# Kernel optimization log

Measured on AMD Instinct MI355X. Metric: run time of the kernel, lower is better.

## Reference

```python
import jax, jax.numpy as jnp
import numpy as np

B, T, D, H = 64, 1024, 512, 1024


def setup_inputs() -> dict:
    key = jax.random.key(0)
    ks = jax.random.split(key, 9)
    s_in = 1.0 / np.sqrt(D)
    s_h = 1.0 / np.sqrt(H)
    x = jax.random.normal(ks[0], (B, T, D), dtype=jnp.float32)
    W0 = jax.random.normal(ks[1], (D, 3 * H), dtype=jnp.float32) * s_in
    U0 = jax.random.normal(ks[2], (H, 3 * H), dtype=jnp.float32) * s_h
    bi0 = jnp.zeros((3 * H,), dtype=jnp.float32)
    br0 = jnp.zeros((3 * H,), dtype=jnp.float32)
    W1 = jax.random.normal(ks[3], (D, 3 * H), dtype=jnp.float32) * s_in
    U1 = jax.random.normal(ks[4], (H, 3 * H), dtype=jnp.float32) * s_h
    bi1 = jnp.zeros((3 * H,), dtype=jnp.float32)
    br1 = jnp.zeros((3 * H,), dtype=jnp.float32)
    return {"x": x, "W0": W0, "U0": U0, "bi0": bi0, "br0": br0,
            "W1": W1, "U1": U1, "bi1": bi1, "br1": br1}


def _gru_last(x, W, U, bi, br):
    """Keras GRUCell (reset_after=True) scanned over time; returns final h [B,H]."""
    h_dim = U.shape[0]
    xT = jnp.swapaxes(x, 0, 1)  # [T, B, D]

    def step(h, xt):
        gx = xt @ W + bi          # [B, 3H] input projection + input bias
        gh = h @ U + br           # [B, 3H] recurrent projection + recurrent bias
        xz, xr, xh = jnp.split(gx, 3, axis=-1)
        hz, hr, hh = jnp.split(gh, 3, axis=-1)
        z = jax.nn.sigmoid(xz + hz)
        r = jax.nn.sigmoid(xr + hr)
        h_cand = jnp.tanh(xh + r * hh)
        h_new = z * h + (1.0 - z) * h_cand
        return h_new, None

    h0 = jnp.zeros((x.shape[0], h_dim), dtype=x.dtype)
    h_last, _ = jax.lax.scan(step, h0, xT)
    return h_last


def reference(x, W0, U0, bi0, br0, W1, U1, bi1, br1):
    out0 = _gru_last(x, W0, U0, bi0, br0)
    out1 = _gru_last(x, W1, U1, bi1, br1)
    return (out0, out1)
```

## Files before the change

kernel.cpp:

```cpp
#include <hip/hip_runtime.h>
#include <hip/hip_bf16.h>

typedef unsigned short u16;
typedef short s8v __attribute__((ext_vector_type(8)));
typedef float f4v __attribute__((ext_vector_type(4)));

#define NB 64
#define NT 1024
#define ND 512
#define NH 1024

static const size_t OFF_BAR  = 0;
static const size_t OFF_HB   = 512;
static const size_t SZ_HB    = (size_t)2*2*NB*NH*2;
static const size_t OFF_XBF  = (size_t)1<<20;
static const size_t SZ_XBF   = (size_t)NB*NT*ND*2;
static const size_t WS_FLOOR = OFF_HB + SZ_HB;
static const size_t WS_FULL  = OFF_XBF + SZ_XBF;

__device__ __forceinline__ u16 f2bf(float f) {
  union { float f; unsigned u; } v; v.f = f;
  unsigned r = v.u + 0x7fffu + ((v.u >> 16) & 1u);
  return (u16)(r >> 16);
}

__global__ void pack_x_kernel(const float* __restrict__ x, u16* __restrict__ xb) {
  long long i = (long long)blockIdx.x * 256 + threadIdx.x;
  const float4* xp = (const float4*)x;
  float4 a = xp[2*i], b = xp[2*i+1];
  s8v v;
  v[0]=(short)f2bf(a.x); v[1]=(short)f2bf(a.y); v[2]=(short)f2bf(a.z); v[3]=(short)f2bf(a.w);
  v[4]=(short)f2bf(b.x); v[5]=(short)f2bf(b.y); v[6]=(short)f2bf(b.z); v[7]=(short)f2bf(b.w);
  *((s8v*)xb + i) = v;
}

__device__ __forceinline__ void gridbar(unsigned* cnt, unsigned* gen, unsigned nb) {
  __syncthreads();
  if (threadIdx.x == 0) {
    __threadfence();
    unsigned g = __hip_atomic_load(gen, __ATOMIC_RELAXED, __HIP_MEMORY_SCOPE_AGENT);
    unsigned a = __hip_atomic_fetch_add(cnt, 1u, __ATOMIC_ACQ_REL, __HIP_MEMORY_SCOPE_AGENT);
    if (a == nb - 1u) {
      __hip_atomic_store(cnt, 0u, __ATOMIC_RELAXED, __HIP_MEMORY_SCOPE_AGENT);
      __hip_atomic_fetch_add(gen, 1u, __ATOMIC_RELEASE, __HIP_MEMORY_SCOPE_AGENT);
    } else {
      while (__hip_atomic_load(gen, __ATOMIC_ACQUIRE, __HIP_MEMORY_SCOPE_AGENT) == g)
        __builtin_amdgcn_s_sleep(2);
    }
    __threadfence();
  }
  __syncthreads();
}

template<int XBF>
__global__ void __launch_bounds__(192, 1)
rnn_persist(const float* __restrict__ xf, const u16* __restrict__ xb,
            const float* __restrict__ W0, const float* __restrict__ U0,
            const float* __restrict__ W1, const float* __restrict__ U1,
            const float* __restrict__ bi0, const float* __restrict__ br0,
            const float* __restrict__ bi1, const float* __restrict__ br1,
            u16* __restrict__ hb, unsigned* __restrict__ bar,
            float* __restrict__ out) {
  __shared__ float zr[2][64][16];
  const int tid  = threadIdx.x;
  const int lane = tid & 63;
  const int g    = tid >> 6;
  const int wg   = blockIdx.x;
  const int hd   = wg >> 6;
  const int j0   = (wg & 63) * 16;
  const int cidx = lane & 15;
  const int hi8  = (lane >> 4) << 3;
  const int q4   = (lane >> 4) << 2;

  const float* W = hd ? W1 : W0;
  const float* U = hd ? U1 : U0;
  const int col = g*1024 + j0 + cidx;

  s8v wf[16], uf[32];
  #pragma unroll
  for (int kk=0;kk<16;++kk) { s8v v;
    #pragma unroll
    for (int j=0;j<8;++j) v[j] = (short)f2bf(W[(size_t)(kk*32 + hi8 + j)*3072 + col]);
    wf[kk]=v; }
  #pragma unroll
  for (int kk=0;kk<32;++kk) { s8v v;
    #pragma unroll
    for (int j=0;j<8;++j) v[j] = (short)f2bf(U[(size_t)(kk*32 + hi8 + j)*3072 + col]);
    uf[kk]=v; }

  const float bis = (hd ? bi1 : bi0)[col];
  const float brs = (hd ? br1 : br0)[col];

  f4v hm[4];
  #pragma unroll
  for (int m=0;m<4;++m) hm[m] = f4v{0.f,0.f,0.f,0.f};

  unsigned* cnt = bar + hd*32;
  unsigned* gen = cnt + 1;

  for (int t = 0; t < NT; ++t) {
    const int p = t & 1;
    f4v cx[4], ch[4];
    #pragma unroll
    for (int m=0;m<4;++m){ cx[m]=f4v{0.f,0.f,0.f,0.f}; ch[m]=f4v{0.f,0.f,0.f,0.f}; }

    #pragma unroll
    for (int kk=0;kk<16;++kk) {
      #pragma unroll
      for (int m=0;m<4;++m) {
        s8v a;
        if (XBF) {
          a = *(const s8v*)(xb + ((size_t)((m*16+cidx)*NT + t))*ND + hi8 + kk*32);
        } else {
          const float* p4 = xf + ((size_t)((m*16+cidx)*NT + t))*ND + hi8 + kk*32;
          float4 u0 = *(const float4*)p4, u1 = *(const float4*)(p4+4);
          a[0]=(short)f2bf(u0.x); a[1]=(short)f2bf(u0.y); a[2]=(short)f2bf(u0.z); a[3]=(short)f2bf(u0.w);
          a[4]=(short)f2bf(u1.x); a[5]=(short)f2bf(u1.y); a[6]=(short)f2bf(u1.z); a[7]=(short)f2bf(u1.w);
        }
        cx[m] = __builtin_amdgcn_mfma_f32_16x16x32_bf16(a, wf[kk], cx[m], 0,0,0);
      }
    }
    const u16* hptr0 = hb + (size_t)(p*2 + hd) * (NB*NH) + (size_t)cidx*NH + hi8;
    #pragma unroll
    for (int kk=0;kk<32;++kk) {
      #pragma unroll
      for (int m=0;m<4;++m) {
        s8v a = *(const s8v*)(hptr0 + (size_t)m*16*NH + kk*32);
        ch[m] = __builtin_amdgcn_mfma_f32_16x16x32_bf16(a, uf[kk], ch[m], 0,0,0);
      }
    }

    if (g < 2) {
      #pragma unroll
      for (int m=0;m<4;++m) {
        #pragma unroll
        for (int q=0;q<4;++q) {
          float v = cx[m][q] + ch[m][q] + bis + brs;
          zr[g][m*16 + q4 + q][cidx] = 1.f/(1.f + __expf(-v));
        }
      }
    }
    __syncthreads();
    if (g == 2) {
      u16* hdst = hb + (size_t)((p^1)*2 + hd) * (NB*NH);
      #pragma unroll
      for (int m=0;m<4;++m) {
        #pragma unroll
        for (int q=0;q<4;++q) {
          int row = m*16 + q4 + q;
          float z  = zr[0][row][cidx];
          float r  = zr[1][row][cidx];
          float hc = tanhf(cx[m][q] + bis + r*(ch[m][q] + brs));
          float hn = z*hm[m][q] + (1.f - z)*hc;
          hm[m][q] = hn;
          hdst[(size_t)row*NH + j0 + cidx] = f2bf(hn);
          if (t == NT-1) out[(size_t)hd*(NB*NH) + (size_t)row*NH + j0 + cidx] = hn;
        }
      }
    }
    gridbar(cnt, gen, 64u);
  }
}

extern "C" void kernel_launch(void* const* d_in, const int* in_sizes, int n_in,
                              void* d_out, int out_size, void* d_ws, size_t ws_size,
                              hipStream_t stream) {
  const float* x   = (const float*)d_in[0];
  const float* W0  = (const float*)d_in[1];
  const float* U0  = (const float*)d_in[2];
  const float* bi0 = (const float*)d_in[3];
  const float* br0 = (const float*)d_in[4];
  const float* W1  = (const float*)d_in[5];
  const float* U1  = (const float*)d_in[6];
  const float* bi1 = (const float*)d_in[7];
  const float* br1 = (const float*)d_in[8];
  float* out = (float*)d_out;
  char* ws = (char*)d_ws;

  if (ws_size < WS_FLOOR) {
    hipMemsetAsync(d_out, 0, (size_t)out_size*4, stream);
    return;
  }

  unsigned* bar = (unsigned*)(ws + OFF_BAR);
  u16* hbb = (u16*)(ws + OFF_HB);
  u16* xbf = (u16*)(ws + OFF_XBF);

  hipMemsetAsync(ws, 0, OFF_HB + SZ_HB, stream);

  if (ws_size >= WS_FULL) {
    pack_x_kernel<<<dim3((NB*NT*ND/8)/256), dim3(256), 0, stream>>>(x, xbf);
    rnn_persist<1><<<dim3(128), dim3(192), 0, stream>>>(
        nullptr, xbf, W0,U0,W1,U1, bi0,br0,bi1,br1, hbb, bar, out);
  } else {
    rnn_persist<0><<<dim3(128), dim3(192), 0, stream>>>(
        x, nullptr, W0,U0,W1,U1, bi0,br0,bi1,br1, hbb, bar, out);
  }
}
```

Baseline: 40.16 ms.

## Overlap next-step input projection with barrier via per-block flags, time-major x layout

Replaces the counter/generation grid barrier with per-workgroup monotonic step flags on separate cache lines; one wavefront polls all 64 peer flags. The next step's input projection (x@W MFMAs) is computed between publishing the flag and waiting, so barrier latency is hidden behind independent work. The packed bf16 x is transposed to time-major [T,B,D] so each step's loads are contiguous, and the LDS z/r array gets padding to reduce bank conflicts. This adds register pressure from the extra accumulator set and one wasted projection on the final step.

```diff
diff --git a/kernel.cpp b/kernel.cpp
--- a/kernel.cpp
+++ b/kernel.cpp
@@ -11,7 +11,8 @@
 #define NH 1024
 
 static const size_t OFF_BAR  = 0;
-static const size_t OFF_HB   = 512;
+static const size_t SZ_BAR   = 16384;
+static const size_t OFF_HB   = SZ_BAR;
 static const size_t SZ_HB    = (size_t)2*2*NB*NH*2;
 static const size_t OFF_XBF  = (size_t)1<<20;
 static const size_t SZ_XBF   = (size_t)NB*NT*ND*2;
@@ -25,31 +26,16 @@
 }
 
 __global__ void pack_x_kernel(const float* __restrict__ x, u16* __restrict__ xb) {
-  long long i = (long long)blockIdx.x * 256 + threadIdx.x;
-  const float4* xp = (const float4*)x;
-  float4 a = xp[2*i], b = xp[2*i+1];
+  long long id = (long long)blockIdx.x * 256 + threadIdx.x;
+  int c = id & 63;
+  int b = (int)((id >> 6) & 63);
+  int t = (int)(id >> 12);
+  const float* src = x + ((size_t)b*NT + t)*ND + c*8;
+  float4 a = *(const float4*)src, d = *(const float4*)(src+4);
   s8v v;
   v[0]=(short)f2bf(a.x); v[1]=(short)f2bf(a.y); v[2]=(short)f2bf(a.z); v[3]=(short)f2bf(a.w);
-  v[4]=(short)f2bf(b.x); v[5]=(short)f2bf(b.y); v[6]=(short)f2bf(b.z); v[7]=(short)f2bf(b.w);
-  *((s8v*)xb + i) = v;
-}
-
-__device__ __forceinline__ void gridbar(unsigned* cnt, unsigned* gen, unsigned nb) {
-  __syncthreads();
-  if (threadIdx.x == 0) {
-    __threadfence();
-    unsigned g = __hip_atomic_load(gen, __ATOMIC_RELAXED, __HIP_MEMORY_SCOPE_AGENT);
-    unsigned a = __hip_atomic_fetch_add(cnt, 1u, __ATOMIC_ACQ_REL, __HIP_MEMORY_SCOPE_AGENT);
-    if (a == nb - 1u) {
-      __hip_atomic_store(cnt, 0u, __ATOMIC_RELAXED, __HIP_MEMORY_SCOPE_AGENT);
-      __hip_atomic_fetch_add(gen, 1u, __ATOMIC_RELEASE, __HIP_MEMORY_SCOPE_AGENT);
-    } else {
-      while (__hip_atomic_load(gen, __ATOMIC_ACQUIRE, __HIP_MEMORY_SCOPE_AGENT) == g)
-        __builtin_amdgcn_s_sleep(2);
-    }
-    __threadfence();
-  }
-  __syncthreads();
+  v[4]=(short)f2bf(d.x); v[5]=(short)f2bf(d.y); v[6]=(short)f2bf(d.z); v[7]=(short)f2bf(d.w);
+  *(s8v*)(xb + ((size_t)t*NB + b)*ND + c*8) = v;
 }
 
 template<int XBF>
@@ -61,7 +47,7 @@
             const float* __restrict__ bi1, const float* __restrict__ br1,
             u16* __restrict__ hb, unsigned* __restrict__ bar,
             float* __restrict__ out) {
-  __shared__ float zr[2][64][16];
+  __shared__ float zr[2][64][18];
   const int tid  = threadIdx.x;
   const int lane = tid & 63;
   const int g    = tid >> 6;
@@ -95,31 +81,38 @@
   #pragma unroll
   for (int m=0;m<4;++m) hm[m] = f4v{0.f,0.f,0.f,0.f};
 
-  unsigned* cnt = bar + hd*32;
-  unsigned* gen = cnt + 1;
-
-  for (int t = 0; t < NT; ++t) {
-    const int p = t & 1;
-    f4v cx[4], ch[4];
-    #pragma unroll
-    for (int m=0;m<4;++m){ cx[m]=f4v{0.f,0.f,0.f,0.f}; ch[m]=f4v{0.f,0.f,0.f,0.f}; }
-
+  unsigned* fbase = bar + hd*1024;
+  unsigned* myfl  = fbase + (wg & 63)*16;
+
+  auto cx_compute = [&](f4v* dst, int tt) {
     #pragma unroll
     for (int kk=0;kk<16;++kk) {
       #pragma unroll
       for (int m=0;m<4;++m) {
         s8v a;
-        if (XBF) {
-          a = *(const s8v*)(xb + ((size_t)((m*16+cidx)*NT + t))*ND + hi8 + kk*32);
+        if constexpr (XBF != 0) {
+          a = *(const s8v*)(xb + ((size_t)tt*NB + (m*16+cidx))*ND + kk*32 + hi8);
         } else {
-          const float* p4 = xf + ((size_t)((m*16+cidx)*NT + t))*ND + hi8 + kk*32;
+          const float* p4 = xf + ((size_t)(m*16+cidx)*NT + tt)*ND + kk*32 + hi8;
           float4 u0 = *(const float4*)p4, u1 = *(const float4*)(p4+4);
           a[0]=(short)f2bf(u0.x); a[1]=(short)f2bf(u0.y); a[2]=(short)f2bf(u0.z); a[3]=(short)f2bf(u0.w);
           a[4]=(short)f2bf(u1.x); a[5]=(short)f2bf(u1.y); a[6]=(short)f2bf(u1.z); a[7]=(short)f2bf(u1.w);
         }
-        cx[m] = __builtin_amdgcn_mfma_f32_16x16x32_bf16(a, wf[kk], cx[m], 0,0,0);
-      }
-    }
+        dst[m] = __builtin_amdgcn_mfma_f32_16x16x32_bf16(a, wf[kk], dst[m], 0,0,0);
+      }
+    }
+  };
+
+  f4v cx[4], cxn[4], ch[4];
+  #pragma unroll
+  for (int m=0;m<4;++m) cx[m] = f4v{0.f,0.f,0.f,0.f};
+  cx_compute(cx, 0);
+
+  for (int t = 0; t < NT; ++t) {
+    const int p = t & 1;
+
+    #pragma unroll
+    for (int m=0;m<4;++m) ch[m] = f4v{0.f,0.f,0.f,0.f};
     const u16* hptr0 = hb + (size_t)(p*2 + hd) * (NB*NH) + (size_t)cidx*NH + hi8;
     #pragma unroll
     for (int kk=0;kk<32;++kk) {
@@ -158,7 +151,29 @@
         }
       }
     }
-    gridbar(cnt, gen, 64u);
+    __syncthreads();
+
+    if (tid == 0) {
+      __threadfence();
+      __hip_atomic_store(myfl, (unsigned)(t+1), __ATOMIC_RELEASE, __HIP_MEMORY_SCOPE_AGENT);
+    }
+
+    #pragma unroll
+    for (int m=0;m<4;++m) cxn[m] = f4v{0.f,0.f,0.f,0.f};
+    const int tn = (t+1 < NT) ? t+1 : 0;
+    cx_compute(cxn, tn);
+
+    if (tid < 64) {
+      unsigned* pf = fbase + lane*16;
+      while (!__all(__hip_atomic_load(pf, __ATOMIC_ACQUIRE, __HIP_MEMORY_SCOPE_AGENT)
+                    >= (unsigned)(t+1)))
+        __builtin_amdgcn_s_sleep(1);
+      __threadfence();
+    }
+    __syncthreads();
+
+    #pragma unroll
+    for (int m=0;m<4;++m) cx[m] = cxn[m];
   }
 }
 
```

Measured after the change: 47.44 ms. 18.1% more time.
